# Optimization experiments

Hardware: AMD Instinct MI355X
Metric: run time of the kernel (lower is better)

## Reference

```python
import jax, jax.numpy as jnp
import numpy as np

FEATURE_DIM = 64
VALUE_DIM = 64
BATCH_HEADS = 64
SEQ_LEN = 4096


def setup_inputs() -> dict:
    key = jax.random.key(0)
    kq, kk, kv = jax.random.split(key, 3)
    q = jax.random.normal(kq, (BATCH_HEADS, SEQ_LEN, FEATURE_DIM), dtype=jnp.float32)
    k = jax.random.normal(kk, (BATCH_HEADS, SEQ_LEN, FEATURE_DIM), dtype=jnp.float32)
    v = jax.random.normal(kv, (BATCH_HEADS, SEQ_LEN, VALUE_DIM), dtype=jnp.float32)
    return {"q": q, "k": k, "v": v}


def reference(q, k, v):
    # q,k: (BH, S, F); v: (BH, S, V)
    # Recurrence: w_t = w_{t-1} + k_t v_t^T ; out_t = (q_t . w_t) / (t+1)
    bh, seq_len, f = q.shape
    val = v.shape[-1]

    def step(w, qkv_t):
        q_t, k_t, v_t = qkv_t  # (BH,F), (BH,F), (BH,V)
        w = w + jnp.einsum('bf,bv->bfv', k_t, v_t)
        out_t = jnp.einsum('bf,bfv->bv', q_t, w)
        return w, out_t

    w0 = jnp.zeros((bh, f, val), dtype=q.dtype)
    # scan over the sequence axis (time-major)
    xs = (jnp.swapaxes(q, 0, 1), jnp.swapaxes(k, 0, 1), jnp.swapaxes(v, 0, 1))
    _, outs = jax.lax.scan(step, w0, xs)  # outs: (S, BH, V)
    denom = jnp.arange(1, seq_len + 1, dtype=q.dtype)[:, None, None]
    outs = outs / denom
    return jnp.swapaxes(outs, 0, 1)  # (BH, S, V)
```

## Files before the change

kernel.cpp:

```cpp
#include <hip/hip_runtime.h>


#define BH   64
#define SEQ  4096
#define FD   64
#define VD   64
#define C    128
#define NCH  (SEQ / C)

typedef __attribute__((ext_vector_type(8))) short  short8;
typedef __attribute__((ext_vector_type(4))) float  f32x4;

static __device__ __forceinline__ unsigned short f2bf(float f) {
    unsigned int u = __builtin_bit_cast(unsigned int, f);
    u += 0x7FFF + ((u >> 16) & 1);
    return (unsigned short)(u >> 16);
}
static __device__ __forceinline__ float bf2f(unsigned short h) {
    unsigned int u = ((unsigned int)h) << 16;
    return __builtin_bit_cast(float, u);
}
static __device__ __forceinline__ unsigned int pk2(float lo, float hi) {
    unsigned int a = __builtin_bit_cast(unsigned int, lo);
    unsigned int b = __builtin_bit_cast(unsigned int, hi);
    a += 0x7FFF + ((a >> 16) & 1);
    b += 0x7FFF + ((b >> 16) & 1);
    return (a >> 16) | (b & 0xFFFF0000u);
}

__global__ __launch_bounds__(512, 4) void ttr_sums(const float* __restrict__ k,
                                                   const float* __restrict__ v,
                                                   unsigned short* __restrict__ ST) {
    const int b  = blockIdx.x >> 5;
    const int ci = blockIdx.x & 31;
    __shared__ unsigned short KT[64][136];
    __shared__ unsigned short VT[64][136];
    __shared__ unsigned short Cs[64][72];
    const int tid = threadIdx.x;
    const float* kc = k + ((size_t)b * SEQ + (size_t)ci * C) * FD;
    const float* vc = v + ((size_t)b * SEQ + (size_t)ci * C) * FD;

    #pragma unroll
    for (int it = 0; it < 4; ++it) {
        const int i = tid + it * 512;
        const int f = i & 63, t4 = (i >> 6) << 2;
        float k0 = kc[(t4+0)*FD + f], k1 = kc[(t4+1)*FD + f];
        float k2 = kc[(t4+2)*FD + f], k3 = kc[(t4+3)*FD + f];
        float v0 = vc[(t4+0)*FD + f], v1 = vc[(t4+1)*FD + f];
        float v2 = vc[(t4+2)*FD + f], v3 = vc[(t4+3)*FD + f];
        uint2 kw, vw;
        kw.x = pk2(k0, k1); kw.y = pk2(k2, k3);
        vw.x = pk2(v0, v1); vw.y = pk2(v2, v3);
        *(uint2*)&KT[f][t4] = kw;
        *(uint2*)&VT[f][t4] = vw;
    }
    __syncthreads();

    const int wid  = tid >> 6;
    const int lane = tid & 63;
    const int mrow = lane & 15;
    const int kb   = (lane >> 4) << 3;

    if (wid < 4) {
        f32x4 acc[4] = {};
        #pragma unroll
        for (int ks = 0; ks < 4; ++ks) {
            short8 a = *(const short8*)&VT[16 * wid + mrow][ks * 32 + kb];
            #pragma unroll
            for (int cf = 0; cf < 4; ++cf) {
                short8 bb = *(const short8*)&KT[16 * cf + mrow][ks * 32 + kb];
                acc[cf] = __builtin_amdgcn_mfma_f32_16x16x32_bf16(a, bb, acc[cf], 0, 0, 0);
            }
        }
        const int vrow0 = 16 * wid + ((lane >> 4) << 2);
        const int fcol  = lane & 15;
        #pragma unroll
        for (int cf = 0; cf < 4; ++cf)
            #pragma unroll
            for (int r = 0; r < 4; ++r)
                Cs[vrow0 + r][cf * 16 + fcol] = f2bf(acc[cf][r]);
    }
    __syncthreads();

    unsigned short* outp = ST + (size_t)(b * NCH + ci) * (VD * FD);
    const int rr = tid >> 3, c8 = (tid & 7) << 3;
    *(uint4*)(outp + rr * FD + c8) = *(const uint4*)&Cs[rr][c8];
}

__global__ __launch_bounds__(512, 4) void ttr_main(const float* __restrict__ q,
                                                   const float* __restrict__ k,
                                                   const float* __restrict__ v,
                                                   const unsigned short* __restrict__ ST,
                                                   float* __restrict__ out) {
    const unsigned bid = blockIdx.x;
    const int b  = (int)(((bid & 7u) << 3) | (bid >> 8));
    const int ci = (int)((bid >> 3) & 31u);

    __shared__ unsigned short POOL[8 * 16 * 136];
    __shared__ unsigned short Qs[128][72];
    __shared__ unsigned short VTs[64][200];
    const int tid = threadIdx.x;
    const float* qc = q + ((size_t)b * SEQ + (size_t)ci * C) * FD;
    const float* kc = k + ((size_t)b * SEQ + (size_t)ci * C) * FD;
    const float* vc = v + ((size_t)b * SEQ + (size_t)ci * C) * FD;

    {
        float wa[8] = {0.f, 0.f, 0.f, 0.f, 0.f, 0.f, 0.f, 0.f};
        const unsigned short* stb = ST + (size_t)b * NCH * (VD * FD) + tid * 8;
        for (int cj = 0; cj < ci; ++cj) {
            short8 s = *(const short8*)(stb + (size_t)cj * (VD * FD));
            #pragma unroll
            for (int j = 0; j < 8; ++j) wa[j] += bf2f((unsigned short)s[j]);
        }
        const int vv = tid >> 3, f0 = (tid & 7) << 3;
        uint4 wv;
        wv.x = pk2(wa[0], wa[1]); wv.y = pk2(wa[2], wa[3]);
        wv.z = pk2(wa[4], wa[5]); wv.w = pk2(wa[6], wa[7]);
        *(uint4*)&VTs[vv][128 + f0] = wv;
    }

    #pragma unroll
    for (int it = 0; it < 2; ++it) {
        const int i = tid + it * 512;
        const int t = i >> 3, f8 = (i & 7) << 3;
        float4 q0 = *(const float4*)(qc + t * FD + f8);
        float4 q1 = *(const float4*)(qc + t * FD + f8 + 4);
        float4 k0 = *(const float4*)(kc + t * FD + f8);
        float4 k1 = *(const float4*)(kc + t * FD + f8 + 4);
        uint4 qw, kw;
        qw.x = pk2(q0.x, q0.y); qw.y = pk2(q0.z, q0.w);
        qw.z = pk2(q1.x, q1.y); qw.w = pk2(q1.z, q1.w);
        kw.x = pk2(k0.x, k0.y); kw.y = pk2(k0.z, k0.w);
        kw.z = pk2(k1.x, k1.y); kw.w = pk2(k1.z, k1.w);
        *(uint4*)&Qs[t][f8] = qw;
        *(uint4*)&POOL[t * 72 + f8] = kw;
    }

    #pragma unroll
    for (int it = 0; it < 4; ++it) {
        const int i = tid + it * 512;
        const int f = i & 63, t4 = (i >> 6) << 2;
        float v0 = vc[(t4+0)*FD + f], v1 = vc[(t4+1)*FD + f];
        float v2 = vc[(t4+2)*FD + f], v3 = vc[(t4+3)*FD + f];
        uint2 vw;
        vw.x = pk2(v0, v1); vw.y = pk2(v2, v3);
        *(uint2*)&VTs[f][t4] = vw;
    }
    __syncthreads();

    const int wid  = tid >> 6;
    const int lane = tid & 63;
    const int mrow = lane & 15;
    const int kb   = (lane >> 4) << 3;

    f32x4 pacc[8] = {};
    #pragma unroll
    for (int ks = 0; ks < 2; ++ks) {
        short8 a = *(const short8*)&Qs[16 * wid + mrow][ks * 32 + kb];
        #pragma unroll
        for (int cf = 0; cf < 8; ++cf) {
            short8 bb = *(const short8*)&POOL[(16 * cf + mrow) * 72 + ks * 32 + kb];
            pacc[cf] = __builtin_amdgcn_mfma_f32_16x16x32_bf16(a, bb, pacc[cf], 0, 0, 0);
        }
    }
    __syncthreads();

    const int prow0 = (lane >> 4) << 2;
    const int pcol  = lane & 15;
    #pragma unroll
    for (int cf = 0; cf < 8; ++cf)
        #pragma unroll
        for (int r = 0; r < 4; ++r) {
            const int row_local = 16 * wid + prow0 + r;
            const int col       = 16 * cf + pcol;
            const float val = (col <= row_local) ? pacc[cf][r] : 0.f;
            POOL[(16 * wid + prow0 + r) * 136 + col] = f2bf(val);
        }
    __syncthreads();

    f32x4 oacc[4] = {};
    #pragma unroll
    for (int ks = 0; ks < 6; ++ks) {
        short8 a;
        if (ks < 4) a = *(const short8*)&POOL[(16 * wid + mrow) * 136 + ks * 32 + kb];
        else        a = *(const short8*)&Qs[16 * wid + mrow][(ks - 4) * 32 + kb];
        #pragma unroll
        for (int cn = 0; cn < 4; ++cn) {
            short8 bb = *(const short8*)&VTs[16 * cn + mrow][ks * 32 + kb];
            oacc[cn] = __builtin_amdgcn_mfma_f32_16x16x32_bf16(a, bb, oacc[cn], 0, 0, 0);
        }
    }

    float* oc = out + ((size_t)b * SEQ + (size_t)ci * C) * VD;
    #pragma unroll
    for (int cn = 0; cn < 4; ++cn)
        #pragma unroll
        for (int r = 0; r < 4; ++r) {
            const int row_local = 16 * wid + prow0 + r;
            const float den = (float)(ci * C + row_local + 1);
            oc[(size_t)row_local * VD + cn * 16 + pcol] = oacc[cn][r] / den;
        }
}

extern "C" void kernel_launch(void* const* d_in, const int* in_sizes, int n_in,
                              void* d_out, int out_size, void* d_ws, size_t ws_size,
                              hipStream_t stream) {
    const float* q = (const float*)d_in[0];
    const float* k = (const float*)d_in[1];
    const float* v = (const float*)d_in[2];
    float* out = (float*)d_out;
    unsigned short* ST = (unsigned short*)d_ws;

    ttr_sums<<<BH * NCH, 512, 0, stream>>>(k, v, ST);
    ttr_main<<<BH * NCH, 512, 0, stream>>>(q, k, v, ST, out);
}
```

Baseline: 262.1 us.

## Precompute exclusive prefix of chunk states in separate kernel

Adds a small kernel that turns the per-chunk KV outer-product sums into exclusive prefix sums in place, so each main-kernel block reads one precomputed state instead of summing all earlier chunks. This removes the quadratic re-reading of chunk states, where later chunks read up to 31 prior states. It adds a third launch and a serial scan over 32 chunks run by only 128 blocks, so that kernel has little parallelism.

```diff
diff --git a/kernel.cpp b/kernel.cpp
--- a/kernel.cpp
+++ b/kernel.cpp
@@ -87,10 +87,29 @@
     *(uint4*)(outp + rr * FD + c8) = *(const uint4*)&Cs[rr][c8];
 }
 
+__global__ __launch_bounds__(256) void ttr_prefix(unsigned short* __restrict__ ST) {
+    const int gtid = blockIdx.x * 256 + threadIdx.x;
+    const int b    = gtid >> 9;
+    const int off  = (gtid & 511) << 3;
+    unsigned short* p = ST + (size_t)b * NCH * (VD * FD) + off;
+    float acc[8] = {0.f, 0.f, 0.f, 0.f, 0.f, 0.f, 0.f, 0.f};
+    #pragma unroll 8
+    for (int ci = 0; ci < NCH; ++ci) {
+        unsigned short* pc = p + (size_t)ci * (VD * FD);
+        short8 s = *(const short8*)pc;
+        uint4 w;
+        w.x = pk2(acc[0], acc[1]); w.y = pk2(acc[2], acc[3]);
+        w.z = pk2(acc[4], acc[5]); w.w = pk2(acc[6], acc[7]);
+        *(uint4*)pc = w;
+        #pragma unroll
+        for (int j = 0; j < 8; ++j) acc[j] += bf2f((unsigned short)s[j]);
+    }
+}
+
 __global__ __launch_bounds__(512, 4) void ttr_main(const float* __restrict__ q,
                                                    const float* __restrict__ k,
                                                    const float* __restrict__ v,
-                                                   const unsigned short* __restrict__ ST,
+                                                   const unsigned short* __restrict__ WT,
                                                    float* __restrict__ out) {
     const unsigned bid = blockIdx.x;
     const int b  = (int)(((bid & 7u) << 3) | (bid >> 8));
@@ -105,18 +124,9 @@
     const float* vc = v + ((size_t)b * SEQ + (size_t)ci * C) * FD;
 
     {
-        float wa[8] = {0.f, 0.f, 0.f, 0.f, 0.f, 0.f, 0.f, 0.f};
-        const unsigned short* stb = ST + (size_t)b * NCH * (VD * FD) + tid * 8;
-        for (int cj = 0; cj < ci; ++cj) {
-            short8 s = *(const short8*)(stb + (size_t)cj * (VD * FD));
-            #pragma unroll
-            for (int j = 0; j < 8; ++j) wa[j] += bf2f((unsigned short)s[j]);
-        }
+        const unsigned short* wsrc = WT + (size_t)(b * NCH + ci) * (VD * FD);
         const int vv = tid >> 3, f0 = (tid & 7) << 3;
-        uint4 wv;
-        wv.x = pk2(wa[0], wa[1]); wv.y = pk2(wa[2], wa[3]);
-        wv.z = pk2(wa[4], wa[5]); wv.w = pk2(wa[6], wa[7]);
-        *(uint4*)&VTs[vv][128 + f0] = wv;
+        *(uint4*)&VTs[vv][128 + f0] = *(const uint4*)(wsrc + tid * 8);
     }
 
     #pragma unroll
@@ -212,5 +222,6 @@
     unsigned short* ST = (unsigned short*)d_ws;
 
     ttr_sums<<<BH * NCH, 512, 0, stream>>>(k, v, ST);
+    ttr_prefix<<<128, 256, 0, stream>>>(ST);
     ttr_main<<<BH * NCH, 512, 0, stream>>>(q, k, v, ST, out);
 }
```

Result: faster. 245.4 us (-6.3%).
